# Kernel optimization log

Measured on AMD Instinct MI355X. Metric: run time of the kernel, lower is better.

The kernel has to match this reference:

```python
import jax, jax.numpy as jnp
import numpy as np

EMB_DIM = 1024
HEAD_SIZE = 64
SEQ = 2048
BATCH = 8


def setup_inputs() -> dict:
    key = jax.random.key(0)
    kx, kq, kk, kv = jax.random.split(key, 4)
    x = jax.random.normal(kx, (BATCH, SEQ, EMB_DIM), dtype=jnp.float32)
    # nn.Linear(E, H, bias=False): y = x @ W.T with W of shape [H, E]; store as [E, H]
    s = 1.0 / np.sqrt(EMB_DIM)
    Wq = jax.random.uniform(kq, (EMB_DIM, HEAD_SIZE), jnp.float32, -s, s)
    Wk = jax.random.uniform(kk, (EMB_DIM, HEAD_SIZE), jnp.float32, -s, s)
    Wv = jax.random.uniform(kv, (EMB_DIM, HEAD_SIZE), jnp.float32, -s, s)
    return {"x": x, "Wq": Wq, "Wk": Wk, "Wv": Wv}


def reference(x, Wq, Wk, Wv):
    B, S, E = x.shape
    q = jnp.einsum("bse,eh->bsh", x, Wq)
    k = jnp.einsum("bse,eh->bsh", x, Wk)
    v = jnp.einsum("bse,eh->bsh", x, Wv)
    # NOTE: original scales by E**-0.5 (embedding dim), not head_size**-0.5
    att = jnp.einsum("bqh,bkh->bqk", q, k) * (E ** -0.5)
    causal = jnp.tril(jnp.ones((S, S), dtype=bool))
    att = jnp.where(causal, att, -jnp.inf)
    att = jax.nn.softmax(att, axis=-1)
    # dropout(p=0.2) treated as identity (eval mode) for deterministic reference
    out = jnp.einsum("bqk,bkh->bqh", att, v)
    return out
```

## Files before the change

kernel.cpp:

```cpp
#include <hip/hip_runtime.h>

constexpr int Bn = 8, S = 2048, E = 1024, H = 64;
constexpr float SCALE = 0.03125f * 1.44269504f;

typedef __attribute__((ext_vector_type(8))) short short8;
typedef __attribute__((ext_vector_type(4))) float f32x4;

__device__ __forceinline__ unsigned short f2bf(float f) {
  unsigned u = __builtin_bit_cast(unsigned, f);
  u += 0x7fffu + ((u >> 16) & 1u);
  return (unsigned short)(u >> 16);
}
__device__ __forceinline__ ushort4 f4bf(float4 f) {
  return make_ushort4(f2bf(f.x), f2bf(f.y), f2bf(f.z), f2bf(f.w));
}

__global__ __launch_bounds__(256) void wtrans_kernel(
    const float* __restrict__ Wq, const float* __restrict__ Wk,
    const float* __restrict__ Wv, unsigned short* __restrict__ WT3) {
  __shared__ unsigned short tb[64][72];
  const int m = blockIdx.x >> 4;
  const int e0 = (blockIdx.x & 15) * 64;
  const float* W = (m == 0) ? Wq : (m == 1) ? Wk : Wv;
  const int t = threadIdx.x;
#pragma unroll
  for (int it = 0; it < 4; ++it) {
    int idx = t + it * 256;
    int r = idx >> 4, c4 = idx & 15;
    float4 f = ((const float4*)(W + (long)(e0 + r) * H))[c4];
    *(ushort4*)&tb[r][c4 * 4] = f4bf(f);
  }
  __syncthreads();
#pragma unroll
  for (int it = 0; it < 4; ++it) {
    int idx = t + it * 256;
    int h = idx >> 4, e4 = idx & 15;
    ushort4 u = make_ushort4(tb[e4 * 4 + 0][h], tb[e4 * 4 + 1][h],
                             tb[e4 * 4 + 2][h], tb[e4 * 4 + 3][h]);
    ((ushort4*)(WT3 + (long)(m * 64 + h) * E + e0))[e4] = u;
  }
}

__global__ __launch_bounds__(256) void qkv_kernel(
    const float* __restrict__ x, const unsigned short* __restrict__ WT3,
    unsigned short* __restrict__ q, unsigned short* __restrict__ kk,
    unsigned short* __restrict__ vT) {
  __shared__ unsigned short xs[32][136];
  __shared__ unsigned short ws[192][136];
  const int t = threadIdx.x;
  const int w = t >> 6, lane = t & 63, l15 = lane & 15, g = lane >> 4;
  const long row0 = (long)blockIdx.x * 32;
  const int xrow = t >> 5, xslot = t & 31;
  const int wrow = t >> 4, wslot = t & 15;

  f32x4 acc[2][3];
#pragma unroll
  for (int rt = 0; rt < 2; ++rt)
#pragma unroll
    for (int ct = 0; ct < 3; ++ct) acc[rt][ct] = f32x4{0.f, 0.f, 0.f, 0.f};

  float4 px[4];
  short8 pw[12];
#pragma unroll
  for (int it = 0; it < 4; ++it)
    px[it] = ((const float4*)(x + (row0 + xrow + it * 8) * E))[xslot];
#pragma unroll
  for (int it = 0; it < 12; ++it)
    pw[it] = *(const short8*)(WT3 + (long)(wrow + it * 16) * E + wslot * 8);
#pragma unroll
  for (int it = 0; it < 4; ++it)
    *(ushort4*)&xs[xrow + it * 8][xslot * 4] = f4bf(px[it]);
#pragma unroll
  for (int it = 0; it < 12; ++it)
    *(short8*)&ws[wrow + it * 16][wslot * 8] = pw[it];

  for (int c = 0; c < 8; ++c) {
    __syncthreads();
    if (c < 7) {
      const int e0 = (c + 1) * 128;
#pragma unroll
      for (int it = 0; it < 4; ++it)
        px[it] = ((const float4*)(x + (row0 + xrow + it * 8) * E + e0))[xslot];
#pragma unroll
      for (int it = 0; it < 12; ++it)
        pw[it] = *(const short8*)(WT3 + (long)(wrow + it * 16) * E + e0 + wslot * 8);
    }
#pragma unroll
    for (int kh = 0; kh < 4; ++kh) {
      short8 a0 = *(const short8*)&xs[l15][kh * 32 + g * 8];
      short8 a1 = *(const short8*)&xs[16 + l15][kh * 32 + g * 8];
#pragma unroll
      for (int ct = 0; ct < 3; ++ct) {
        short8 b = *(const short8*)&ws[w * 48 + ct * 16 + l15][kh * 32 + g * 8];
        acc[0][ct] = __builtin_amdgcn_mfma_f32_16x16x32_bf16(a0, b, acc[0][ct], 0, 0, 0);
        acc[1][ct] = __builtin_amdgcn_mfma_f32_16x16x32_bf16(a1, b, acc[1][ct], 0, 0, 0);
      }
    }
    __syncthreads();
    if (c < 7) {
#pragma unroll
      for (int it = 0; it < 4; ++it)
        *(ushort4*)&xs[xrow + it * 8][xslot * 4] = f4bf(px[it]);
#pragma unroll
      for (int it = 0; it < 12; ++it)
        *(short8*)&ws[wrow + it * 16][wslot * 8] = pw[it];
    }
  }

  const int bb = (int)(row0 >> 11);
  const int srow = (int)(row0 & 2047);
#pragma unroll
  for (int ct = 0; ct < 3; ++ct) {
    const int col = w * 48 + ct * 16 + l15;
    const int mm = col >> 6, ch = col & 63;
#pragma unroll
    for (int rt = 0; rt < 2; ++rt) {
      const int srl = rt * 16 + g * 4;
      if (mm == 0) {
#pragma unroll
        for (int r = 0; r < 4; ++r)
          q[(row0 + srl + r) * H + ch] = f2bf(acc[rt][ct][r] * SCALE);
      } else if (mm == 1) {
#pragma unroll
        for (int r = 0; r < 4; ++r)
          kk[(row0 + srl + r) * H + ch] = f2bf(acc[rt][ct][r]);
      } else {
        ushort4 v4 = make_ushort4(f2bf(acc[rt][ct][0]), f2bf(acc[rt][ct][1]),
                                  f2bf(acc[rt][ct][2]), f2bf(acc[rt][ct][3]));
        *(ushort4*)(vT + ((long)bb * H + ch) * S + srow + srl) = v4;
      }
    }
  }
}

__global__ __launch_bounds__(512) void attn_kernel(
    const unsigned short* __restrict__ q, const unsigned short* __restrict__ k,
    const unsigned short* __restrict__ vT, float* __restrict__ out) {
  __shared__ unsigned short Kl[2][64][64];
  __shared__ unsigned short Vl[2][64][64];
  __shared__ unsigned short pl[8][16][72];
  const int t = threadIdx.x;
  const int w = t >> 6, lane = t & 63, l15 = lane & 15, g = lane >> 4;
  const int b = blockIdx.x & 7, qb = blockIdx.x >> 3;
  const int r0 = qb * 128;
  const int ntile = 2 * qb + 2;
  const int myNt = 2 * qb + (w >> 2) + 1;
  const int qrow = r0 + w * 16 + l15;
  const unsigned short* kb = k + (long)b * S * H;
  const unsigned short* vb = vT + (long)b * H * S;

  const int srow = t >> 3, scol = t & 7;
  const int swz = (scol ^ (srow & 7)) * 8;

  short8 bq0, bq1;
  {
    const unsigned short* qp = q + ((long)b * S + qrow) * H + g * 8;
    bq0 = *(const short8*)qp;
    bq1 = *(const short8*)(qp + 32);
  }
  f32x4 O[4];
#pragma unroll
  for (int c = 0; c < 4; ++c) O[c] = f32x4{0.f, 0.f, 0.f, 0.f};
  float m_ = -1e30f, l_ = 0.f;

  const int rc0 = (g ^ (l15 & 7)) * 8;
  const int rc1 = ((4 + g) ^ (l15 & 7)) * 8;

  {
    uint4 pk = *(const uint4*)(kb + ((long)srow << 6) + scol * 8);
    uint4 pv = *(const uint4*)(vb + (long)srow * S + scol * 8);
    *(uint4*)&Kl[0][srow][swz] = pk;
    *(uint4*)&Vl[0][srow][swz] = pv;
    __syncthreads();
  }

  for (int kt = 0; kt < ntile; ++kt) {
    const int cur = kt & 1;
    const int k0 = kt * 64;
    const bool pf = (kt + 1 < ntile);
    uint4 pk, pv;
    if (pf) {
      const int kn = k0 + 64;
      pk = *(const uint4*)(kb + ((long)(kn + srow) << 6) + scol * 8);
      pv = *(const uint4*)(vb + (long)srow * S + kn + scol * 8);
    }
    if (kt < myNt) {
      short8 ak[4][2];
#pragma unroll
      for (int c = 0; c < 4; ++c) {
        ak[c][0] = *(const short8*)&Kl[cur][c * 16 + l15][rc0];
        ak[c][1] = *(const short8*)&Kl[cur][c * 16 + l15][rc1];
      }
      f32x4 sc[4];
#pragma unroll
      for (int c = 0; c < 4; ++c) {
        sc[c] = f32x4{0.f, 0.f, 0.f, 0.f};
        sc[c] = __builtin_amdgcn_mfma_f32_16x16x32_bf16(ak[c][0], bq0, sc[c], 0, 0, 0);
        sc[c] = __builtin_amdgcn_mfma_f32_16x16x32_bf16(ak[c][1], bq1, sc[c], 0, 0, 0);
      }
      if (kt == myNt - 1) {
#pragma unroll
        for (int c = 0; c < 4; ++c)
#pragma unroll
          for (int r = 0; r < 4; ++r)
            if (k0 + c * 16 + g * 4 + r > qrow) sc[c][r] = -1e30f;
      }
      float x0 = fmaxf(fmaxf(sc[0][0], sc[0][1]), fmaxf(sc[0][2], sc[0][3]));
      float x1 = fmaxf(fmaxf(sc[1][0], sc[1][1]), fmaxf(sc[1][2], sc[1][3]));
      float x2 = fmaxf(fmaxf(sc[2][0], sc[2][1]), fmaxf(sc[2][2], sc[2][3]));
      float x3 = fmaxf(fmaxf(sc[3][0], sc[3][1]), fmaxf(sc[3][2], sc[3][3]));
      float pmax = fmaxf(fmaxf(x0, x1), fmaxf(x2, x3));
      if (!__all(pmax - m_ <= 10.0f)) {
        float mx = fmaxf(pmax, __shfl_xor(pmax, 16));
        mx = fmaxf(mx, __shfl_xor(mx, 32));
        float mn = fmaxf(m_, mx);
        float al = exp2f(m_ - mn);
        l_ *= al;
#pragma unroll
        for (int c = 0; c < 4; ++c)
#pragma unroll
          for (int r = 0; r < 4; ++r) O[c][r] *= al;
        m_ = mn;
      }
#pragma unroll
      for (int c = 0; c < 4; ++c)
#pragma unroll
        for (int r = 0; r < 4; ++r) sc[c][r] = exp2f(sc[c][r] - m_);
      float s0 = (sc[0][0] + sc[0][1]) + (sc[0][2] + sc[0][3]);
      float s1 = (sc[1][0] + sc[1][1]) + (sc[1][2] + sc[1][3]);
      float s2 = (sc[2][0] + sc[2][1]) + (sc[2][2] + sc[2][3]);
      float s3 = (sc[3][0] + sc[3][1]) + (sc[3][2] + sc[3][3]);
      l_ += (s0 + s1) + (s2 + s3);
#pragma unroll
      for (int c = 0; c < 4; ++c) {
        ushort4 p4 = make_ushort4(f2bf(sc[c][0]), f2bf(sc[c][1]),
                                  f2bf(sc[c][2]), f2bf(sc[c][3]));
        *(ushort4*)&pl[w][l15][c * 16 + g * 4] = p4;
      }
      short8 bp0 = *(const short8*)&pl[w][l15][g * 8];
      short8 bp1 = *(const short8*)&pl[w][l15][32 + g * 8];
#pragma unroll
      for (int c = 0; c < 4; ++c) {
        short8 av0 = *(const short8*)&Vl[cur][c * 16 + l15][rc0];
        short8 av1 = *(const short8*)&Vl[cur][c * 16 + l15][rc1];
        O[c] = __builtin_amdgcn_mfma_f32_16x16x32_bf16(av0, bp0, O[c], 0, 0, 0);
        O[c] = __builtin_amdgcn_mfma_f32_16x16x32_bf16(av1, bp1, O[c], 0, 0, 0);
      }
    }
    if (pf) {
      *(uint4*)&Kl[cur ^ 1][srow][swz] = pk;
      *(uint4*)&Vl[cur ^ 1][srow][swz] = pv;
    }
    __syncthreads();
  }

  l_ += __shfl_xor(l_, 16);
  l_ += __shfl_xor(l_, 32);
  const float inv = 1.0f / l_;
  float* op = out + ((long)b * S + qrow) * H + g * 4;
#pragma unroll
  for (int c = 0; c < 4; ++c)
    *(float4*)(op + c * 16) = make_float4(O[c][0] * inv, O[c][1] * inv,
                                          O[c][2] * inv, O[c][3] * inv);
}

extern "C" void kernel_launch(void* const* d_in, const int* in_sizes, int n_in,
                              void* d_out, int out_size, void* d_ws, size_t ws_size,
                              hipStream_t stream) {
  const float* x  = (const float*)d_in[0];
  const float* Wq = (const float*)d_in[1];
  const float* Wk = (const float*)d_in[2];
  const float* Wv = (const float*)d_in[3];
  float* outp = (float*)d_out;
  unsigned short* WT3 = (unsigned short*)d_ws;
  unsigned short* q  = (unsigned short*)((char*)d_ws + 512 * 1024);
  unsigned short* kk = q + (size_t)Bn * S * H;
  unsigned short* vT = kk + (size_t)Bn * S * H;
  wtrans_kernel<<<dim3(48), dim3(256), 0, stream>>>(Wq, Wk, Wv, WT3);
  qkv_kernel<<<dim3((Bn * S) / 32), dim3(256), 0, stream>>>(x, WT3, q, kk, vT);
  attn_kernel<<<dim3(Bn * 16), dim3(512), 0, stream>>>(q, kk, vT, outp);
}
```

Before: 150.2 us.

## Use direct global-to-LDS loads with pre-swizzled K/V and smaller attention blocks

The QKV kernel now writes K and V^T in an XOR-swizzled layout, so the attention kernel can stage tiles with global_load_lds straight into shared memory, with no register round-trip. The attention kernel goes from 128 blocks of 512 threads (128 query rows) to 512 blocks of 128 threads (32 query rows). Blocks are issued heaviest-first, which balances the causal workload and fills more CUs. K/V loads are double-buffered two tiles ahead using explicit vmcnt waits and barriers. In exchange, each K/V tile is reloaded by four times as many blocks, and the hand-written waitcnt and barrier logic is fragile.

```diff
diff --git a/kernel.cpp b/kernel.cpp
--- a/kernel.cpp
+++ b/kernel.cpp
@@ -13,6 +13,12 @@
 }
 __device__ __forceinline__ ushort4 f4bf(float4 f) {
   return make_ushort4(f2bf(f.x), f2bf(f.y), f2bf(f.z), f2bf(f.w));
+}
+
+__device__ __forceinline__ void glds16(const unsigned short* g, unsigned short* l) {
+  __builtin_amdgcn_global_load_lds(
+      (const __attribute__((address_space(1))) unsigned int*)g,
+      (__attribute__((address_space(3))) unsigned int*)l, 16, 0, 0);
 }
 
 __global__ __launch_bounds__(256) void wtrans_kernel(
@@ -122,35 +128,39 @@
           q[(row0 + srl + r) * H + ch] = f2bf(acc[rt][ct][r] * SCALE);
       } else if (mm == 1) {
 #pragma unroll
-        for (int r = 0; r < 4; ++r)
-          kk[(row0 + srl + r) * H + ch] = f2bf(acc[rt][ct][r]);
+        for (int r = 0; r < 4; ++r) {
+          int gr = (int)(row0 + srl + r);
+          int hsw = (((ch >> 3) ^ (gr & 7)) << 3) | (ch & 7);
+          kk[(long)gr * H + hsw] = f2bf(acc[rt][ct][r]);
+        }
       } else {
         ushort4 v4 = make_ushort4(f2bf(acc[rt][ct][0]), f2bf(acc[rt][ct][1]),
                                   f2bf(acc[rt][ct][2]), f2bf(acc[rt][ct][3]));
-        *(ushort4*)(vT + ((long)bb * H + ch) * S + srow + srl) = v4;
+        long kbase = srow + srl;
+        int k6 = (int)kbase & 63;
+        int kgrp = (k6 >> 3) ^ (ch & 7);
+        long vaddr = ((long)bb * H + ch) * S + (kbase & ~63L) + (kgrp << 3) + (k6 & 7);
+        *(ushort4*)(vT + vaddr) = v4;
       }
     }
   }
 }
 
-__global__ __launch_bounds__(512) void attn_kernel(
+__global__ __launch_bounds__(128) void attn_kernel(
     const unsigned short* __restrict__ q, const unsigned short* __restrict__ k,
     const unsigned short* __restrict__ vT, float* __restrict__ out) {
   __shared__ unsigned short Kl[2][64][64];
   __shared__ unsigned short Vl[2][64][64];
-  __shared__ unsigned short pl[8][16][72];
+  __shared__ unsigned short pl[2][16][72];
   const int t = threadIdx.x;
   const int w = t >> 6, lane = t & 63, l15 = lane & 15, g = lane >> 4;
-  const int b = blockIdx.x & 7, qb = blockIdx.x >> 3;
-  const int r0 = qb * 128;
-  const int ntile = 2 * qb + 2;
-  const int myNt = 2 * qb + (w >> 2) + 1;
-  const int qrow = r0 + w * 16 + l15;
+  const int b = blockIdx.x & 7, j = blockIdx.x >> 3;
+  const int qb = 63 - j;
+  const int nt = (qb >> 1) + 1;
+  const int qrow = qb * 32 + w * 16 + l15;
+  const int sx = l15 & 7;
   const unsigned short* kb = k + (long)b * S * H;
   const unsigned short* vb = vT + (long)b * H * S;
-
-  const int srow = t >> 3, scol = t & 7;
-  const int swz = (scol ^ (srow & 7)) * 8;
 
   short8 bq0, bq1;
   {
@@ -163,95 +173,91 @@
   for (int c = 0; c < 4; ++c) O[c] = f32x4{0.f, 0.f, 0.f, 0.f};
   float m_ = -1e30f, l_ = 0.f;
 
-  const int rc0 = (g ^ (l15 & 7)) * 8;
-  const int rc1 = ((4 + g) ^ (l15 & 7)) * 8;
-
-  {
-    uint4 pk = *(const uint4*)(kb + ((long)srow << 6) + scol * 8);
-    uint4 pv = *(const uint4*)(vb + (long)srow * S + scol * 8);
-    *(uint4*)&Kl[0][srow][swz] = pk;
-    *(uint4*)&Vl[0][srow][swz] = pv;
-    __syncthreads();
-  }
-
-  for (int kt = 0; kt < ntile; ++kt) {
+  auto STAGE = [&](int kt2, int buf) {
+    const unsigned short* kg = kb + (long)(kt2 * 64 + w * 32) * H + lane * 8;
+    const unsigned short* vg = vb + (long)(w * 32 + (lane >> 3)) * S + kt2 * 64 + (lane & 7) * 8;
+    unsigned short* kl = &Kl[buf][w * 32][0];
+    unsigned short* vl = &Vl[buf][w * 32][0];
+#pragma unroll
+    for (int i = 0; i < 4; ++i) {
+      glds16(kg + i * 512, kl + i * 512);
+      glds16(vg + (long)i * 8 * S, vl + i * 512);
+    }
+  };
+
+  STAGE(0, 0);
+  if (nt > 1) STAGE(1, 1);
+
+  for (int kt = 0; kt < nt; ++kt) {
+    if (kt + 1 < nt) { asm volatile("s_waitcnt vmcnt(8)" ::: "memory"); }
+    else             { asm volatile("s_waitcnt vmcnt(0)" ::: "memory"); }
+    __builtin_amdgcn_sched_barrier(0);
+    __builtin_amdgcn_s_barrier();
     const int cur = kt & 1;
     const int k0 = kt * 64;
-    const bool pf = (kt + 1 < ntile);
-    uint4 pk, pv;
-    if (pf) {
-      const int kn = k0 + 64;
-      pk = *(const uint4*)(kb + ((long)(kn + srow) << 6) + scol * 8);
-      pv = *(const uint4*)(vb + (long)srow * S + kn + scol * 8);
-    }
-    if (kt < myNt) {
-      short8 ak[4][2];
-#pragma unroll
-      for (int c = 0; c < 4; ++c) {
-        ak[c][0] = *(const short8*)&Kl[cur][c * 16 + l15][rc0];
-        ak[c][1] = *(const short8*)&Kl[cur][c * 16 + l15][rc1];
-      }
-      f32x4 sc[4];
-#pragma unroll
-      for (int c = 0; c < 4; ++c) {
-        sc[c] = f32x4{0.f, 0.f, 0.f, 0.f};
-        sc[c] = __builtin_amdgcn_mfma_f32_16x16x32_bf16(ak[c][0], bq0, sc[c], 0, 0, 0);
-        sc[c] = __builtin_amdgcn_mfma_f32_16x16x32_bf16(ak[c][1], bq1, sc[c], 0, 0, 0);
-      }
-      if (kt == myNt - 1) {
-#pragma unroll
-        for (int c = 0; c < 4; ++c)
-#pragma unroll
-          for (int r = 0; r < 4; ++r)
-            if (k0 + c * 16 + g * 4 + r > qrow) sc[c][r] = -1e30f;
-      }
-      float x0 = fmaxf(fmaxf(sc[0][0], sc[0][1]), fmaxf(sc[0][2], sc[0][3]));
-      float x1 = fmaxf(fmaxf(sc[1][0], sc[1][1]), fmaxf(sc[1][2], sc[1][3]));
-      float x2 = fmaxf(fmaxf(sc[2][0], sc[2][1]), fmaxf(sc[2][2], sc[2][3]));
-      float x3 = fmaxf(fmaxf(sc[3][0], sc[3][1]), fmaxf(sc[3][2], sc[3][3]));
-      float pmax = fmaxf(fmaxf(x0, x1), fmaxf(x2, x3));
-      if (!__all(pmax - m_ <= 10.0f)) {
-        float mx = fmaxf(pmax, __shfl_xor(pmax, 16));
-        mx = fmaxf(mx, __shfl_xor(mx, 32));
-        float mn = fmaxf(m_, mx);
-        float al = exp2f(m_ - mn);
-        l_ *= al;
-#pragma unroll
-        for (int c = 0; c < 4; ++c)
-#pragma unroll
-          for (int r = 0; r < 4; ++r) O[c][r] *= al;
-        m_ = mn;
-      }
+    short8 ak[4][2], av[4][2];
+#pragma unroll
+    for (int c = 0; c < 4; ++c) {
+      ak[c][0] = *(const short8*)&Kl[cur][c * 16 + l15][(g ^ sx) * 8];
+      ak[c][1] = *(const short8*)&Kl[cur][c * 16 + l15][((4 + g) ^ sx) * 8];
+      av[c][0] = *(const short8*)&Vl[cur][c * 16 + l15][(g ^ sx) * 8];
+      av[c][1] = *(const short8*)&Vl[cur][c * 16 + l15][((4 + g) ^ sx) * 8];
+    }
+    f32x4 sc[4];
+#pragma unroll
+    for (int c = 0; c < 4; ++c) {
+      sc[c] = f32x4{0.f, 0.f, 0.f, 0.f};
+      sc[c] = __builtin_amdgcn_mfma_f32_16x16x32_bf16(ak[c][0], bq0, sc[c], 0, 0, 0);
+      sc[c] = __builtin_amdgcn_mfma_f32_16x16x32_bf16(ak[c][1], bq1, sc[c], 0, 0, 0);
+    }
+    if (kt == nt - 1) {
 #pragma unroll
       for (int c = 0; c < 4; ++c)
 #pragma unroll
-        for (int r = 0; r < 4; ++r) sc[c][r] = exp2f(sc[c][r] - m_);
-      float s0 = (sc[0][0] + sc[0][1]) + (sc[0][2] + sc[0][3]);
-      float s1 = (sc[1][0] + sc[1][1]) + (sc[1][2] + sc[1][3]);
-      float s2 = (sc[2][0] + sc[2][1]) + (sc[2][2] + sc[2][3]);
-      float s3 = (sc[3][0] + sc[3][1]) + (sc[3][2] + sc[3][3]);
-      l_ += (s0 + s1) + (s2 + s3);
-#pragma unroll
-      for (int c = 0; c < 4; ++c) {
-        ushort4 p4 = make_ushort4(f2bf(sc[c][0]), f2bf(sc[c][1]),
-                                  f2bf(sc[c][2]), f2bf(sc[c][3]));
-        *(ushort4*)&pl[w][l15][c * 16 + g * 4] = p4;
-      }
-      short8 bp0 = *(const short8*)&pl[w][l15][g * 8];
-      short8 bp1 = *(const short8*)&pl[w][l15][32 + g * 8];
-#pragma unroll
-      for (int c = 0; c < 4; ++c) {
-        short8 av0 = *(const short8*)&Vl[cur][c * 16 + l15][rc0];
-        short8 av1 = *(const short8*)&Vl[cur][c * 16 + l15][rc1];
-        O[c] = __builtin_amdgcn_mfma_f32_16x16x32_bf16(av0, bp0, O[c], 0, 0, 0);
-        O[c] = __builtin_amdgcn_mfma_f32_16x16x32_bf16(av1, bp1, O[c], 0, 0, 0);
-      }
-    }
-    if (pf) {
-      *(uint4*)&Kl[cur ^ 1][srow][swz] = pk;
-      *(uint4*)&Vl[cur ^ 1][srow][swz] = pv;
-    }
-    __syncthreads();
+        for (int r = 0; r < 4; ++r)
+          if (k0 + c * 16 + g * 4 + r > qrow) sc[c][r] = -1e30f;
+    }
+    float x0 = fmaxf(fmaxf(sc[0][0], sc[0][1]), fmaxf(sc[0][2], sc[0][3]));
+    float x1 = fmaxf(fmaxf(sc[1][0], sc[1][1]), fmaxf(sc[1][2], sc[1][3]));
+    float x2 = fmaxf(fmaxf(sc[2][0], sc[2][1]), fmaxf(sc[2][2], sc[2][3]));
+    float x3 = fmaxf(fmaxf(sc[3][0], sc[3][1]), fmaxf(sc[3][2], sc[3][3]));
+    float pmax = fmaxf(fmaxf(x0, x1), fmaxf(x2, x3));
+    if (!__all(pmax - m_ <= 10.0f)) {
+      float mx = fmaxf(pmax, __shfl_xor(pmax, 16));
+      mx = fmaxf(mx, __shfl_xor(mx, 32));
+      float mn = fmaxf(m_, mx);
+      float al = exp2f(m_ - mn);
+      l_ *= al;
+#pragma unroll
+      for (int c = 0; c < 4; ++c)
+#pragma unroll
+        for (int r = 0; r < 4; ++r) O[c][r] *= al;
+      m_ = mn;
+    }
+#pragma unroll
+    for (int c = 0; c < 4; ++c)
+#pragma unroll
+      for (int r = 0; r < 4; ++r) sc[c][r] = exp2f(sc[c][r] - m_);
+    float s0 = (sc[0][0] + sc[0][1]) + (sc[0][2] + sc[0][3]);
+    float s1 = (sc[1][0] + sc[1][1]) + (sc[1][2] + sc[1][3]);
+    float s2 = (sc[2][0] + sc[2][1]) + (sc[2][2] + sc[2][3]);
+    float s3 = (sc[3][0] + sc[3][1]) + (sc[3][2] + sc[3][3]);
+    l_ += (s0 + s1) + (s2 + s3);
+#pragma unroll
+    for (int c = 0; c < 4; ++c) {
+      ushort4 p4 = make_ushort4(f2bf(sc[c][0]), f2bf(sc[c][1]),
+                                f2bf(sc[c][2]), f2bf(sc[c][3]));
+      *(ushort4*)&pl[w][l15][c * 16 + g * 4] = p4;
+    }
+    short8 bp0 = *(const short8*)&pl[w][l15][g * 8];
+    short8 bp1 = *(const short8*)&pl[w][l15][32 + g * 8];
+#pragma unroll
+    for (int c = 0; c < 4; ++c) {
+      O[c] = __builtin_amdgcn_mfma_f32_16x16x32_bf16(av[c][0], bp0, O[c], 0, 0, 0);
+      O[c] = __builtin_amdgcn_mfma_f32_16x16x32_bf16(av[c][1], bp1, O[c], 0, 0, 0);
+    }
+    __builtin_amdgcn_s_barrier();
+    if (kt + 2 < nt) STAGE(kt + 2, cur);
   }
 
   l_ += __shfl_xor(l_, 16);
@@ -278,5 +284,5 @@
   unsigned short* vT = kk + (size_t)Bn * S * H;
   wtrans_kernel<<<dim3(48), dim3(256), 0, stream>>>(Wq, Wk, Wv, WT3);
   qkv_kernel<<<dim3((Bn * S) / 32), dim3(256), 0, stream>>>(x, WT3, q, kk, vT);
-  attn_kernel<<<dim3(Bn * 16), dim3(512), 0, stream>>>(q, kk, vT, outp);
-}
+  attn_kernel<<<dim3(Bn * 64), dim3(128), 0, stream>>>(q, kk, vT, outp);
+}
```

Result: no change. 150.8 us (+0.4%).
